# Kernel tuning notes

Hardware: AMD Instinct MI355X
Metric: run time of the kernel (lower is better)

The kernel has to match this reference:

```python
import jax, jax.numpy as jnp
import numpy as np

EPS = 1e-12  # F.normalize eps


def _l2norm(x):
    n = jnp.sqrt(jnp.sum(x * x, axis=-1, keepdims=True))
    return x / jnp.maximum(n, EPS)


def setup_inputs() -> dict:
    key = jax.random.key(0)
    k1, k2, k3 = jax.random.split(key, 3)
    B, C, D = 512, 100000, 128
    batch = jax.random.normal(k1, (B, D), dtype=jnp.float32)
    labels = jax.random.randint(k2, (B,), 0, C, dtype=jnp.int64)
    proxies = jax.random.normal(k3, (C, D), dtype=jnp.float32) / 8
    return {"batch": batch, "labels": labels, "proxies": proxies}


def reference(batch, labels, proxies):
    # batch: [B, D], labels: [B] int, proxies: [C, D]
    x = 3.0 * _l2norm(batch)          # [B, D]
    p = 3.0 * _l2norm(proxies)        # [C, D]
    x2 = jnp.sum(x * x, axis=1, keepdims=True)       # [B, 1]
    p2 = jnp.sum(p * p, axis=1)[None, :]             # [1, C]
    dist = x2 + p2 - 2.0 * jnp.einsum("bd,cd->bc", x, p)  # [B, C]
    B = batch.shape[0]
    pos_dist = dist[jnp.arange(B), labels]           # [B]
    # logsumexp(-dist) over negatives only: mask out positive class
    is_pos = labels[:, None] == jnp.arange(proxies.shape[0])[None, :]  # [B, C]
    neg_scores = jnp.where(is_pos, -jnp.inf, -dist)
    neg_lse = jax.nn.logsumexp(neg_scores, axis=1)   # [B]
    return jnp.mean(pos_dist + neg_lse)
```

## Files before the change

### kernel.cpp

```cpp
#include <hip/hip_runtime.h>
#include <hip/hip_bf16.h>
#include <math.h>

#define B_ 512
#define C_ 100000
#define D_ 128
#define SC 64
#define NSTEP ((C_ + SC - 1) / SC)
#define NPAD (NSTEP * SC - C_)
#define GRID_MAIN 256
#define LOG2E 1.4426950408889634f
#define K2S (2.0f * LOG2E)
#define K18S (-18.0f * LOG2E)

typedef __attribute__((ext_vector_type(8))) short short8;
typedef __attribute__((ext_vector_type(4))) float f32x4;

__device__ __forceinline__ unsigned short f2b(float x) {
  union { float f; unsigned int i; } v; v.f = x;
  unsigned int r = v.i + 0x7FFFu + ((v.i >> 16) & 1u);
  return (unsigned short)(r >> 16);
}
__device__ __forceinline__ float b2f(unsigned short u) {
  union { float f; unsigned int i; } v; v.i = ((unsigned int)u) << 16; return v.f;
}

#if defined(__has_builtin)
#if __has_builtin(__builtin_amdgcn_exp2f)
#define EXP2F(x) __builtin_amdgcn_exp2f(x)
#endif
#endif
#ifndef EXP2F
#define EXP2F(x) __expf(0.69314718055994531f * (x))
#endif

__device__ __forceinline__ void gll16(const void* g, void* l) {
  __builtin_amdgcn_global_load_lds(
      (const __attribute__((address_space(1))) void*)g,
      (__attribute__((address_space(3))) void*)l, 16, 0, 0);
}

__global__ __launch_bounds__(256) void batch_norm_kernel(
    const float* __restrict__ batch, unsigned short* __restrict__ xnb)
{
  int lane = threadIdx.x & 63, wv = threadIdx.x >> 6;
  int r = blockIdx.x * 4 + wv;
  float2 v = *(const float2*)(batch + (size_t)r * D_ + lane * 2);
  float ss = v.x * v.x + v.y * v.y;
#pragma unroll
  for (int off = 32; off; off >>= 1) ss += __shfl_xor(ss, off);
  float sc = 3.f / fmaxf(sqrtf(ss), 1e-12f);
  ushort2 o; o.x = f2b(v.x * sc); o.y = f2b(v.y * sc);
  *(ushort2*)(xnb + (size_t)r * D_ + lane * 2) = o;
}

__global__ __launch_bounds__(512, 2) void pnca_main_kernel(
    const float* __restrict__ praw, const unsigned short* __restrict__ xnb,
    float* __restrict__ pt)
{
  __shared__ __align__(16) float         fbuf[2][SC * D_];
  __shared__ __align__(16) unsigned char bbuf[2][SC * D_ * 2];

  const int tid  = threadIdx.x;
  const int lane = tid & 63;
  const int w    = tid >> 6;
  const int ll   = lane & 15;
  const int lq   = lane >> 4;
  const int st0  = blockIdx.x;

  short8 a[4][4];
#pragma unroll
  for (int m = 0; m < 4; ++m)
#pragma unroll
    for (int ks = 0; ks < 4; ++ks)
      a[m][ks] = *(const short8*)(xnb + (size_t)(w * 64 + m * 16 + ll) * D_ + ks * 32 + lq * 8);

  float part[4][4];
#pragma unroll
  for (int m = 0; m < 4; ++m)
#pragma unroll
    for (int r = 0; r < 4; ++r) part[m][r] = 0.f;

  auto STAGE = [&](int st, int pp) {
    const unsigned char* gb = (const unsigned char*)praw;
#pragma unroll
    for (int k = 0; k < 4; ++k) {
      int slot = k * 512 + tid;
      int gr   = st * SC + (slot >> 5);
      if (gr >= C_) gr = C_ - 1;
      gll16(gb + ((size_t)gr * 32 + (slot & 31)) * 16,
            (unsigned char*)fbuf[pp] + (size_t)(k * 512 + w * 64) * 16);
    }
  };

  auto CVT = [&](int st, int pp) {
    const int c = tid >> 3, j = tid & 7;
    const float* Fb = fbuf[pp] + (size_t)c * D_;
    float x[16]; float ss = 0.f;
#pragma unroll
    for (int i = 0; i < 4; ++i) {
      float4 v = *(const float4*)(Fb + (j + 8 * i) * 4);
      x[4*i+0] = v.x; x[4*i+1] = v.y; x[4*i+2] = v.z; x[4*i+3] = v.w;
      ss += v.x * v.x + v.y * v.y + v.z * v.z + v.w * v.w;
    }
    ss += __shfl_xor(ss, 1);
    ss += __shfl_xor(ss, 2);
    ss += __shfl_xor(ss, 4);
    float sc = (st * SC + c < C_) ? 3.0f * __frsqrt_rn(fmaxf(ss, 1e-24f)) : 0.0f;
    unsigned char* Bb = bbuf[pp];
#pragma unroll
    for (int i = 0; i < 4; ++i) {
      union { unsigned long long q; __hip_bfloat162 h[2]; } u2;
      u2.h[0] = __float22bfloat162_rn(make_float2(x[4*i]   * sc, x[4*i+1] * sc));
      u2.h[1] = __float22bfloat162_rn(make_float2(x[4*i+2] * sc, x[4*i+3] * sc));
      int lu = (j >> 1) + 4 * i;
      int pu = lu ^ (c & 7);
      *(unsigned long long*)(Bb + ((size_t)c * 16 + pu) * 16 + (j & 1) * 8) = u2.q;
    }
  };

  auto COMPUTE = [&](int pp) {
    const unsigned char* Bb = bbuf[pp];
#pragma unroll
    for (int g = 0; g < 4; ++g) {
      const int cg = g * 16 + ll;
      short8 bfr[4];
#pragma unroll
      for (int ks = 0; ks < 4; ++ks)
        bfr[ks] = *(const short8*)(Bb + (size_t)(cg * 16 + ((ks * 4 + lq) ^ (cg & 7))) * 16);
      f32x4 acc[4];
#pragma unroll
      for (int m = 0; m < 4; ++m) acc[m] = (f32x4){0.f, 0.f, 0.f, 0.f};
#pragma unroll
      for (int ks = 0; ks < 4; ++ks)
#pragma unroll
        for (int m = 0; m < 4; ++m)
          acc[m] = __builtin_amdgcn_mfma_f32_16x16x32_bf16(a[m][ks], bfr[ks], acc[m], 0, 0, 0);
#pragma unroll
      for (int m = 0; m < 4; ++m)
#pragma unroll
        for (int r = 0; r < 4; ++r)
          part[m][r] += EXP2F(fmaf(acc[m][r], K2S, K18S));
    }
  };

  STAGE(st0, 0);
  __syncthreads();
  CVT(st0, 0);
  __syncthreads();

  int p = 0;
  for (int st = st0; st < NSTEP; st += GRID_MAIN) {
    const int stn = st + GRID_MAIN;
    const bool hn = (stn < NSTEP);
    if (hn) STAGE(stn, p ^ 1);
    COMPUTE(p);
    __syncthreads();
    if (hn) CVT(stn, p ^ 1);
    __syncthreads();
    p ^= 1;
  }

#pragma unroll
  for (int m = 0; m < 4; ++m)
#pragma unroll
    for (int r = 0; r < 4; ++r) {
      float v = part[m][r];
      v += __shfl_xor(v, 1);
      v += __shfl_xor(v, 2);
      v += __shfl_xor(v, 4);
      v += __shfl_xor(v, 8);
      if (ll == 0)
        pt[(size_t)blockIdx.x * B_ + w * 64 + m * 16 + lq * 4 + r] = v;
    }
}

__global__ __launch_bounds__(256) void finalize_rows_kernel(
    const float* __restrict__ praw, const unsigned short* __restrict__ xnb,
    const int* __restrict__ labels, const float* __restrict__ pt,
    float* __restrict__ lossb)
{
  int lane = threadIdx.x & 63, wv = threadIdx.x >> 6;
  int row = blockIdx.x * 4 + wv;
  int lab = labels[row];
  float2 pv = *(const float2*)(praw + (size_t)lab * D_ + lane * 2);
  ushort2 xv = *(const ushort2*)(xnb + (size_t)row * D_ + lane * 2);
  float xa = b2f(xv.x), xb = b2f(xv.y);
  float ssp = pv.x * pv.x + pv.y * pv.y;
  float dp  = xa * pv.x + xb * pv.y;
#pragma unroll
  for (int off = 32; off; off >>= 1) {
    ssp += __shfl_xor(ssp, off);
    dp  += __shfl_xor(dp, off);
  }
  float pd = 18.f - 2.f * dp * (3.f / fmaxf(sqrtf(ssp), 1e-12f));
  float s = 0.f;
#pragma unroll
  for (int gg = 0; gg < GRID_MAIN / 64; ++gg)
    s += pt[(size_t)(gg * 64 + lane) * B_ + row];
#pragma unroll
  for (int off = 32; off; off >>= 1) s += __shfl_xor(s, off);
  if (lane == 0) {
    const float tail = (float)NPAD * EXP2F(K18S);
    lossb[row] = pd + logf(s - __expf(-pd) - tail);
  }
}

__global__ __launch_bounds__(512) void reduce_mean_kernel(
    const float* __restrict__ lossb, float* __restrict__ out)
{
  int t = threadIdx.x;
  float v = lossb[t];
#pragma unroll
  for (int off = 1; off < 64; off <<= 1) v += __shfl_xor(v, off);
  __shared__ float red[8];
  if ((t & 63) == 0) red[t >> 6] = v;
  __syncthreads();
  if (t == 0) {
    float tot = 0.f;
    for (int i = 0; i < 8; ++i) tot += red[i];
    out[0] = tot / (float)B_;
  }
}

extern "C" void kernel_launch(void* const* d_in, const int* in_sizes, int n_in,
                              void* d_out, int out_size, void* d_ws, size_t ws_size,
                              hipStream_t stream)
{
  const float* batch   = (const float*)d_in[0];
  const int*   labels  = (const int*)d_in[1];
  const float* proxies = (const float*)d_in[2];
  float* out = (float*)d_out;

  unsigned char* ws = (unsigned char*)d_ws;
  unsigned short* xnb = (unsigned short*)ws;
  float* pt    = (float*)(ws + 131072);
  float* lossb = (float*)(ws + 131072 + (size_t)GRID_MAIN * B_ * 4);

  batch_norm_kernel<<<B_ / 4, 256, 0, stream>>>(batch, xnb);
  pnca_main_kernel<<<GRID_MAIN, 512, 0, stream>>>(proxies, xnb, pt);
  finalize_rows_kernel<<<B_ / 4, 256, 0, stream>>>(proxies, xnb, labels, pt, lossb);
  reduce_mean_kernel<<<1, 512, 0, stream>>>(lossb, out);
}
```

Baseline: 39.88 us.

## Fuse batch normalization into main kernel and deepen proxy prefetch pipeline

Removes the separate batch-normalization launch: each block now loads the raw fp32 batch rows, normalizes them and converts them to bf16 MFMA operands in registers, and the finalize kernel computes the positive distance directly from the raw batch. The main loop also prefetches two stages ahead with manual vmcnt waits and raw s_barriers, so the global-to-LDS load of tile s+2 overlaps the conversion of tile s+1 and the MFMA compute of tile s. This saves one launch and the intermediate round trip, and hides more load latency. In exchange every block redundantly normalizes all 512 batch rows, and the hand-written waitcnt/barrier logic is fragile.

```diff
diff --git a/kernel.cpp b/kernel.cpp
--- a/kernel.cpp
+++ b/kernel.cpp
@@ -16,11 +16,6 @@
 typedef __attribute__((ext_vector_type(8))) short short8;
 typedef __attribute__((ext_vector_type(4))) float f32x4;
 
-__device__ __forceinline__ unsigned short f2b(float x) {
-  union { float f; unsigned int i; } v; v.f = x;
-  unsigned int r = v.i + 0x7FFFu + ((v.i >> 16) & 1u);
-  return (unsigned short)(r >> 16);
-}
 __device__ __forceinline__ float b2f(unsigned short u) {
   union { float f; unsigned int i; } v; v.i = ((unsigned int)u) << 16; return v.f;
 }
@@ -40,22 +35,8 @@
       (__attribute__((address_space(3))) void*)l, 16, 0, 0);
 }
 
-__global__ __launch_bounds__(256) void batch_norm_kernel(
-    const float* __restrict__ batch, unsigned short* __restrict__ xnb)
-{
-  int lane = threadIdx.x & 63, wv = threadIdx.x >> 6;
-  int r = blockIdx.x * 4 + wv;
-  float2 v = *(const float2*)(batch + (size_t)r * D_ + lane * 2);
-  float ss = v.x * v.x + v.y * v.y;
-#pragma unroll
-  for (int off = 32; off; off >>= 1) ss += __shfl_xor(ss, off);
-  float sc = 3.f / fmaxf(sqrtf(ss), 1e-12f);
-  ushort2 o; o.x = f2b(v.x * sc); o.y = f2b(v.y * sc);
-  *(ushort2*)(xnb + (size_t)r * D_ + lane * 2) = o;
-}
-
 __global__ __launch_bounds__(512, 2) void pnca_main_kernel(
-    const float* __restrict__ praw, const unsigned short* __restrict__ xnb,
+    const float* __restrict__ praw, const float* __restrict__ batch,
     float* __restrict__ pt)
 {
   __shared__ __align__(16) float         fbuf[2][SC * D_];
@@ -70,10 +51,31 @@
 
   short8 a[4][4];
 #pragma unroll
-  for (int m = 0; m < 4; ++m)
-#pragma unroll
-    for (int ks = 0; ks < 4; ++ks)
-      a[m][ks] = *(const short8*)(xnb + (size_t)(w * 64 + m * 16 + ll) * D_ + ks * 32 + lq * 8);
+  for (int m = 0; m < 4; ++m) {
+    float4 t0[4], t1[4];
+    float ssm = 0.f;
+#pragma unroll
+    for (int ks = 0; ks < 4; ++ks) {
+      const float* rp = batch + (size_t)(w * 64 + m * 16 + ll) * D_ + ks * 32 + lq * 8;
+      t0[ks] = *(const float4*)rp;
+      t1[ks] = *(const float4*)(rp + 4);
+      ssm += t0[ks].x * t0[ks].x + t0[ks].y * t0[ks].y + t0[ks].z * t0[ks].z + t0[ks].w * t0[ks].w
+           + t1[ks].x * t1[ks].x + t1[ks].y * t1[ks].y + t1[ks].z * t1[ks].z + t1[ks].w * t1[ks].w;
+    }
+    ssm += __shfl_xor(ssm, 16);
+    ssm += __shfl_xor(ssm, 32);
+    float sc = 3.f / fmaxf(sqrtf(ssm), 1e-12f);
+#pragma unroll
+    for (int ks = 0; ks < 4; ++ks) {
+      union { short8 s8; __hip_bfloat162 h[4]; } u;
+      u.h[0] = __float22bfloat162_rn(make_float2(t0[ks].x * sc, t0[ks].y * sc));
+      u.h[1] = __float22bfloat162_rn(make_float2(t0[ks].z * sc, t0[ks].w * sc));
+      u.h[2] = __float22bfloat162_rn(make_float2(t1[ks].x * sc, t1[ks].y * sc));
+      u.h[3] = __float22bfloat162_rn(make_float2(t1[ks].z * sc, t1[ks].w * sc));
+      a[m][ks] = u.s8;
+    }
+  }
+  asm volatile("s_waitcnt vmcnt(0)" ::: "memory");
 
   float part[4][4];
 #pragma unroll
@@ -145,20 +147,30 @@
   };
 
   STAGE(st0, 0);
-  __syncthreads();
+  STAGE(st0 + GRID_MAIN, 1);
+  asm volatile("s_waitcnt vmcnt(4)" ::: "memory");
+  __builtin_amdgcn_s_barrier();
+  __builtin_amdgcn_sched_barrier(0);
   CVT(st0, 0);
-  __syncthreads();
-
-  int p = 0;
+  __builtin_amdgcn_s_barrier();
+
+  int cur = 0;
   for (int st = st0; st < NSTEP; st += GRID_MAIN) {
-    const int stn = st + GRID_MAIN;
-    const bool hn = (stn < NSTEP);
-    if (hn) STAGE(stn, p ^ 1);
-    COMPUTE(p);
-    __syncthreads();
-    if (hn) CVT(stn, p ^ 1);
-    __syncthreads();
-    p ^= 1;
+    const int s1 = st + GRID_MAIN;
+    const int s2 = st + 2 * GRID_MAIN;
+    const bool h1 = (s1 < NSTEP);
+    const bool h2 = (s2 < NSTEP);
+    if (h2) STAGE(s2, cur);
+    if (h1) {
+      if (h2) asm volatile("s_waitcnt vmcnt(4)" ::: "memory");
+      else    asm volatile("s_waitcnt vmcnt(0)" ::: "memory");
+    }
+    __builtin_amdgcn_s_barrier();
+    __builtin_amdgcn_sched_barrier(0);
+    if (h1) CVT(s1, cur ^ 1);
+    COMPUTE(cur);
+    __builtin_amdgcn_s_barrier();
+    cur ^= 1;
   }
 
 #pragma unroll
@@ -176,7 +188,7 @@
 }
 
 __global__ __launch_bounds__(256) void finalize_rows_kernel(
-    const float* __restrict__ praw, const unsigned short* __restrict__ xnb,
+    const float* __restrict__ praw, const float* __restrict__ batch,
     const int* __restrict__ labels, const float* __restrict__ pt,
     float* __restrict__ lossb)
 {
@@ -184,16 +196,17 @@
   int row = blockIdx.x * 4 + wv;
   int lab = labels[row];
   float2 pv = *(const float2*)(praw + (size_t)lab * D_ + lane * 2);
-  ushort2 xv = *(const ushort2*)(xnb + (size_t)row * D_ + lane * 2);
-  float xa = b2f(xv.x), xb = b2f(xv.y);
+  float2 xv = *(const float2*)(batch + (size_t)row * D_ + lane * 2);
   float ssp = pv.x * pv.x + pv.y * pv.y;
-  float dp  = xa * pv.x + xb * pv.y;
+  float ssx = xv.x * xv.x + xv.y * xv.y;
+  float dp  = xv.x * pv.x + xv.y * pv.y;
 #pragma unroll
   for (int off = 32; off; off >>= 1) {
     ssp += __shfl_xor(ssp, off);
+    ssx += __shfl_xor(ssx, off);
     dp  += __shfl_xor(dp, off);
   }
-  float pd = 18.f - 2.f * dp * (3.f / fmaxf(sqrtf(ssp), 1e-12f));
+  float pd = 18.f - 18.f * dp / (fmaxf(sqrtf(ssx), 1e-12f) * fmaxf(sqrtf(ssp), 1e-12f));
   float s = 0.f;
 #pragma unroll
   for (int gg = 0; gg < GRID_MAIN / 64; ++gg)
@@ -233,12 +246,10 @@
   float* out = (float*)d_out;
 
   unsigned char* ws = (unsigned char*)d_ws;
-  unsigned short* xnb = (unsigned short*)ws;
-  float* pt    = (float*)(ws + 131072);
-  float* lossb = (float*)(ws + 131072 + (size_t)GRID_MAIN * B_ * 4);
-
-  batch_norm_kernel<<<B_ / 4, 256, 0, stream>>>(batch, xnb);
-  pnca_main_kernel<<<GRID_MAIN, 512, 0, stream>>>(proxies, xnb, pt);
-  finalize_rows_kernel<<<B_ / 4, 256, 0, stream>>>(proxies, xnb, labels, pt, lossb);
+  float* pt    = (float*)ws;
+  float* lossb = (float*)(ws + (size_t)GRID_MAIN * B_ * 4);
+
+  pnca_main_kernel<<<GRID_MAIN, 512, 0, stream>>>(proxies, batch, pt);
+  finalize_rows_kernel<<<B_ / 4, 256, 0, stream>>>(proxies, batch, labels, pt, lossb);
   reduce_mean_kernel<<<1, 512, 0, stream>>>(lossb, out);
 }
```

Result: no change. 40.54 us (+1.7%).
